# Optimization experiments

Hardware: AMD Instinct MI355X
Metric: run time of the kernel (lower is better)

## Reference

```python
import jax, jax.numpy as jnp
import numpy as np

EPS = 1e-8  # torch.nn.CosineSimilarity default eps


def _one_sided_chamfer(ex, ey):
    # ex: [N, D], ey: [M, D]
    # cosine(ex_i, ey_j) = <ex_i, ey_j> / (max(||ex_i||, eps) * max(||ey_j||, eps))
    nx = jnp.maximum(jnp.linalg.norm(ex, axis=-1, keepdims=True), EPS)  # [N,1]
    ny = jnp.maximum(jnp.linalg.norm(ey, axis=-1, keepdims=True), EPS)  # [M,1]
    exn = ex / nx
    eyn = ey / ny
    sims = jnp.einsum('nd,md->nm', exn, eyn)  # [N, M] cosine matrix
    return jnp.max(sims, axis=-1)  # row-wise max -> [N]


def setup_inputs() -> dict:
    key = jax.random.key(0)
    k1, k2 = jax.random.split(key)
    ex = jax.random.normal(k1, (8192, 768), dtype=jnp.float32)
    ey = jax.random.normal(k2, (8192, 768), dtype=jnp.float32)
    return {"ex": ex, "ey": ey}


def reference(ex, ey):
    return _one_sided_chamfer(ex, ey)
```

## Files before the change

### kernel.cpp

```cpp
#include <hip/hip_runtime.h>
#include <math.h>

#define NROWS 8192
#define KDIM  768
#define BM 128
#define BN 128
#define BKB 128
#define KTILES (KDIM / BKB)
#define NBC 4
#define NBCG (NROWS / BN / NBC)

typedef int i32x4 __attribute__((ext_vector_type(4)));

static __device__ __forceinline__ unsigned enc_f(float f) {
    unsigned x = __float_as_uint(f);
    return (x & 0x80000000u) ? ~x : (x | 0x80000000u);
}
static __device__ __forceinline__ float dec_f(unsigned u) {
    unsigned x = (u & 0x80000000u) ? (u ^ 0x80000000u) : ~u;
    return __uint_as_float(x);
}

__global__ __launch_bounds__(256) void normalize_quant_k(
        const float* __restrict__ ex, const float* __restrict__ ey,
        signed char* __restrict__ q, float* __restrict__ scales,
        unsigned* __restrict__ out) {
    if (blockIdx.x < NROWS / 256)
        out[blockIdx.x * 256 + threadIdx.x] = enc_f(-INFINITY);
    const int wave = threadIdx.x >> 6, lane = threadIdx.x & 63;
    const int grow = blockIdx.x * 4 + wave;
    const float* src = (grow < NROWS) ? ex : ey;
    const int row = grow & (NROWS - 1);
    const float4* xr = (const float4*)(src + (size_t)row * KDIM);
    float4 v[3];
    #pragma unroll
    for (int g = 0; g < 3; ++g) v[g] = xr[lane + g * 64];
    float ss = 0.f, am = 0.f;
    #pragma unroll
    for (int g = 0; g < 3; ++g) {
        ss += v[g].x * v[g].x + v[g].y * v[g].y + v[g].z * v[g].z + v[g].w * v[g].w;
        am = fmaxf(am, fmaxf(fmaxf(fabsf(v[g].x), fabsf(v[g].y)),
                             fmaxf(fabsf(v[g].z), fabsf(v[g].w))));
    }
    #pragma unroll
    for (int off = 32; off > 0; off >>= 1) {
        ss += __shfl_xor(ss, off);
        am = fmaxf(am, __shfl_xor(am, off));
    }
    const float scale = 1.0f / fmaxf(sqrtf(ss), 1e-8f);
    am = fmaxf(am * scale, 1e-12f);
    if (lane == 0) scales[grow] = am * (1.0f / 127.0f);
    const float si = scale * (127.0f / am);
    int* dr = (int*)(q + (size_t)grow * KDIM);
    #pragma unroll
    for (int g = 0; g < 3; ++g) {
        int qx = min(127, max(-127, __float2int_rn(v[g].x * si)));
        int qy = min(127, max(-127, __float2int_rn(v[g].y * si)));
        int qz = min(127, max(-127, __float2int_rn(v[g].z * si)));
        int qw = min(127, max(-127, __float2int_rn(v[g].w * si)));
        dr[lane + g * 64] = (qx & 0xff) | ((qy & 0xff) << 8) |
                            ((qz & 0xff) << 16) | ((qw & 0xff) << 24);
    }
}

__global__ __launch_bounds__(256, 4) void gemm_rowmax_i8_k(
        const signed char* __restrict__ A, const signed char* __restrict__ B,
        const float* __restrict__ sa, const float* __restrict__ sb,
        unsigned* __restrict__ out) {
    __shared__ signed char As[BM * BKB];
    __shared__ signed char Bs[BN * BKB];

    const int tid  = threadIdx.x;
    const int wave = tid >> 6, lane = tid & 63;
    const int br  = blockIdx.x >> 4;
    const int bcg = blockIdx.x & 15;

    const int srow   = lane >> 3;
    const int gchunk = (lane & 7) ^ srow;
    const int scol   = gchunk * 16;
    const signed char* aStage = A + (size_t)(br * BM + wave * 8 + srow) * KDIM + scol;
    signed char* lA = As + wave * 1024;
    signed char* lB = Bs + wave * 1024;

    const int wm = (wave >> 1) * 64, wn = (wave & 1) * 64;
    const int quad = lane >> 4, mrow = lane & 15;
    const int c0 = quad ^ (mrow & 7);
    const signed char* aBase = As + (wm + mrow) * BKB;
    const signed char* bBase = Bs + (wn + mrow) * BKB;
    const int row0 = br * BM + wm + quad * 4;

    #pragma unroll 1
    for (int bi = 0; bi < NBC; ++bi) {
        const int bc = bcg * NBC + bi;
        const signed char* bStage =
            B + (size_t)(bc * BN + wave * 8 + srow) * KDIM + scol;

        i32x4 acc[4][4] = {};

        #pragma unroll 1
        for (int kt = 0; kt < KTILES; ++kt) {
            __syncthreads();
            #pragma unroll
            for (int i = 0; i < 4; ++i) {
                __builtin_amdgcn_global_load_lds(
                    (const __attribute__((address_space(1))) void*)(aStage + kt * BKB + i * 24576),
                    (__attribute__((address_space(3))) void*)(lA + i * 4096), 16, 0, 0);
                __builtin_amdgcn_global_load_lds(
                    (const __attribute__((address_space(1))) void*)(bStage + kt * BKB + i * 24576),
                    (__attribute__((address_space(3))) void*)(lB + i * 4096), 16, 0, 0);
            }
            __syncthreads();

            #pragma unroll 1
            for (int ks = 0; ks < 2; ++ks) {
                const int ck = c0 ^ (ks << 2);
                i32x4 af[4], bfr[4];
                #pragma unroll
                for (int mi = 0; mi < 4; ++mi)
                    af[mi] = *(const i32x4*)(aBase + mi * 16 * BKB + ck * 16);
                #pragma unroll
                for (int ni = 0; ni < 4; ++ni)
                    bfr[ni] = *(const i32x4*)(bBase + ni * 16 * BKB + ck * 16);
                #pragma unroll
                for (int mi = 0; mi < 4; ++mi)
                    #pragma unroll
                    for (int ni = 0; ni < 4; ++ni)
                        acc[mi][ni] = __builtin_amdgcn_mfma_i32_16x16x64_i8(
                            af[mi], bfr[ni], acc[mi][ni], 0, 0, 0);
            }
        }

        float sbv[4];
        #pragma unroll
        for (int ni = 0; ni < 4; ++ni)
            sbv[ni] = sb[bc * BN + wn + ni * 16 + mrow];
        #pragma unroll
        for (int mi = 0; mi < 4; ++mi) {
            #pragma unroll
            for (int r = 0; r < 4; ++r) {
                float v = fmaxf(fmaxf((float)acc[mi][0][r] * sbv[0],
                                      (float)acc[mi][1][r] * sbv[1]),
                                fmaxf((float)acc[mi][2][r] * sbv[2],
                                      (float)acc[mi][3][r] * sbv[3]));
                v = fmaxf(v, __shfl_xor(v, 1));
                v = fmaxf(v, __shfl_xor(v, 2));
                v = fmaxf(v, __shfl_xor(v, 4));
                v = fmaxf(v, __shfl_xor(v, 8));
                if (mrow == 0) {
                    const int row = row0 + mi * 16 + r;
                    atomicMax(&out[row], enc_f(v * sa[row]));
                }
            }
        }
    }
}

__global__ void decode_out_k(unsigned* __restrict__ u) {
    int i = blockIdx.x * 256 + threadIdx.x;
    ((float*)u)[i] = dec_f(u[i]);
}

extern "C" void kernel_launch(void* const* d_in, const int* in_sizes, int n_in,
                              void* d_out, int out_size, void* d_ws, size_t ws_size,
                              hipStream_t stream) {
    (void)in_sizes; (void)n_in; (void)out_size; (void)ws_size;
    const float* ex = (const float*)d_in[0];
    const float* ey = (const float*)d_in[1];
    signed char* q = (signed char*)d_ws;
    float* scales  = (float*)(q + 2 * (size_t)NROWS * KDIM);
    unsigned* outu = (unsigned*)d_out;

    normalize_quant_k<<<(2 * NROWS) / 4, 256, 0, stream>>>(ex, ey, q, scales, outu);
    gemm_rowmax_i8_k<<<(NROWS / BM) * NBCG, 256, 0, stream>>>(
        q, q + (size_t)NROWS * KDIM, scales, scales + NROWS, outu);
    decode_out_k<<<NROWS / 256, 256, 0, stream>>>(outu);
}
```

Measured before the change: 158.0 us.

## Pre-swizzle int8 operands into MFMA fragment layout and load directly from global

The quantize kernel now writes int8 data in a tiled layout that matches the MFMA fragment order: 16-row groups, with each 64-byte k-chunk laid out lane-contiguous. The GEMM kernel drops LDS staging and both barriers per k-tile, and each wave reads its fragments straight from global memory with coalesced 16-byte loads. This removes the LDS round trip and the synchronisation cost. In exchange, operands shared across waves are loaded redundantly from global/L2 and there is no explicit prefetch, so load latency is exposed.

```diff
diff --git a/kernel.cpp b/kernel.cpp
--- a/kernel.cpp
+++ b/kernel.cpp
@@ -5,8 +5,8 @@
 #define KDIM  768
 #define BM 128
 #define BN 128
-#define BKB 128
-#define KTILES (KDIM / BKB)
+#define NCH 12
+#define GBYTES 12288
 #define NBC 4
 #define NBCG (NROWS / BN / NBC)
 
@@ -23,43 +23,51 @@
 
 __global__ __launch_bounds__(256) void normalize_quant_k(
         const float* __restrict__ ex, const float* __restrict__ ey,
-        signed char* __restrict__ q, float* __restrict__ scales,
+        signed char* __restrict__ qt, float* __restrict__ scales,
         unsigned* __restrict__ out) {
-    if (blockIdx.x < NROWS / 256)
-        out[blockIdx.x * 256 + threadIdx.x] = enc_f(-INFINITY);
+    const int b = blockIdx.x;
+    if (b < NROWS / 256)
+        out[b * 256 + threadIdx.x] = enc_f(-INFINITY);
     const int wave = threadIdx.x >> 6, lane = threadIdx.x & 63;
-    const int grow = blockIdx.x * 4 + wave;
-    const float* src = (grow < NROWS) ? ex : ey;
-    const int row = grow & (NROWS - 1);
-    const float4* xr = (const float4*)(src + (size_t)row * KDIM);
-    float4 v[3];
+    const int r_local = wave * 4 + (lane >> 4);
+    const int l16 = lane & 15;
+    const int grow = b * 16 + r_local;
+    const float* src = (b < 512) ? ex : ey;
+    const int Rl = ((b & 511) * 16 + r_local);
+    const float4* xr = (const float4*)(src + (size_t)Rl * KDIM);
+
+    float4 v[NCH];
     #pragma unroll
-    for (int g = 0; g < 3; ++g) v[g] = xr[lane + g * 64];
+    for (int rep = 0; rep < NCH; ++rep) v[rep] = xr[l16 + 16 * rep];
+
     float ss = 0.f, am = 0.f;
     #pragma unroll
-    for (int g = 0; g < 3; ++g) {
-        ss += v[g].x * v[g].x + v[g].y * v[g].y + v[g].z * v[g].z + v[g].w * v[g].w;
-        am = fmaxf(am, fmaxf(fmaxf(fabsf(v[g].x), fabsf(v[g].y)),
-                             fmaxf(fabsf(v[g].z), fabsf(v[g].w))));
+    for (int rep = 0; rep < NCH; ++rep) {
+        ss += v[rep].x * v[rep].x + v[rep].y * v[rep].y +
+              v[rep].z * v[rep].z + v[rep].w * v[rep].w;
+        am = fmaxf(am, fmaxf(fmaxf(fabsf(v[rep].x), fabsf(v[rep].y)),
+                             fmaxf(fabsf(v[rep].z), fabsf(v[rep].w))));
     }
     #pragma unroll
-    for (int off = 32; off > 0; off >>= 1) {
+    for (int off = 1; off < 16; off <<= 1) {
         ss += __shfl_xor(ss, off);
         am = fmaxf(am, __shfl_xor(am, off));
     }
     const float scale = 1.0f / fmaxf(sqrtf(ss), 1e-8f);
     am = fmaxf(am * scale, 1e-12f);
-    if (lane == 0) scales[grow] = am * (1.0f / 127.0f);
+    if (l16 == 0) scales[grow] = am * (1.0f / 127.0f);
     const float si = scale * (127.0f / am);
-    int* dr = (int*)(q + (size_t)grow * KDIM);
+
+    signed char* gbase = qt + (size_t)b * GBYTES
+                       + (l16 >> 2) * 256 + r_local * 16 + (l16 & 3) * 4;
     #pragma unroll
-    for (int g = 0; g < 3; ++g) {
-        int qx = min(127, max(-127, __float2int_rn(v[g].x * si)));
-        int qy = min(127, max(-127, __float2int_rn(v[g].y * si)));
-        int qz = min(127, max(-127, __float2int_rn(v[g].z * si)));
-        int qw = min(127, max(-127, __float2int_rn(v[g].w * si)));
-        dr[lane + g * 64] = (qx & 0xff) | ((qy & 0xff) << 8) |
-                            ((qz & 0xff) << 16) | ((qw & 0xff) << 24);
+    for (int rep = 0; rep < NCH; ++rep) {
+        int qx = min(127, max(-127, __float2int_rn(v[rep].x * si)));
+        int qy = min(127, max(-127, __float2int_rn(v[rep].y * si)));
+        int qz = min(127, max(-127, __float2int_rn(v[rep].z * si)));
+        int qw = min(127, max(-127, __float2int_rn(v[rep].w * si)));
+        *(int*)(gbase + rep * 1024) =
+            (qx & 0xff) | ((qy & 0xff) << 8) | ((qz & 0xff) << 16) | ((qw & 0xff) << 24);
     }
 }
 
@@ -67,73 +75,47 @@
         const signed char* __restrict__ A, const signed char* __restrict__ B,
         const float* __restrict__ sa, const float* __restrict__ sb,
         unsigned* __restrict__ out) {
-    __shared__ signed char As[BM * BKB];
-    __shared__ signed char Bs[BN * BKB];
-
     const int tid  = threadIdx.x;
     const int wave = tid >> 6, lane = tid & 63;
     const int br  = blockIdx.x >> 4;
     const int bcg = blockIdx.x & 15;
 
-    const int srow   = lane >> 3;
-    const int gchunk = (lane & 7) ^ srow;
-    const int scol   = gchunk * 16;
-    const signed char* aStage = A + (size_t)(br * BM + wave * 8 + srow) * KDIM + scol;
-    signed char* lA = As + wave * 1024;
-    signed char* lB = Bs + wave * 1024;
+    const int wgA = (wave >> 1) * 4;
+    const int wgB = (wave & 1) * 4;
+    const size_t laneoff = (size_t)lane * 16;
 
-    const int wm = (wave >> 1) * 64, wn = (wave & 1) * 64;
+    const signed char* aT = A + (size_t)(br * 8 + wgA) * GBYTES + laneoff;
     const int quad = lane >> 4, mrow = lane & 15;
-    const int c0 = quad ^ (mrow & 7);
-    const signed char* aBase = As + (wm + mrow) * BKB;
-    const signed char* bBase = Bs + (wn + mrow) * BKB;
-    const int row0 = br * BM + wm + quad * 4;
+    const int row0 = br * BM + wgA * 16 + quad * 4;
 
     #pragma unroll 1
     for (int bi = 0; bi < NBC; ++bi) {
         const int bc = bcg * NBC + bi;
-        const signed char* bStage =
-            B + (size_t)(bc * BN + wave * 8 + srow) * KDIM + scol;
+        const signed char* bT = B + (size_t)(bc * 8 + wgB) * GBYTES + laneoff;
 
         i32x4 acc[4][4] = {};
 
         #pragma unroll 1
-        for (int kt = 0; kt < KTILES; ++kt) {
-            __syncthreads();
+        for (int c = 0; c < NCH; ++c) {
+            i32x4 af[4], bfr[4];
             #pragma unroll
-            for (int i = 0; i < 4; ++i) {
-                __builtin_amdgcn_global_load_lds(
-                    (const __attribute__((address_space(1))) void*)(aStage + kt * BKB + i * 24576),
-                    (__attribute__((address_space(3))) void*)(lA + i * 4096), 16, 0, 0);
-                __builtin_amdgcn_global_load_lds(
-                    (const __attribute__((address_space(1))) void*)(bStage + kt * BKB + i * 24576),
-                    (__attribute__((address_space(3))) void*)(lB + i * 4096), 16, 0, 0);
-            }
-            __syncthreads();
-
-            #pragma unroll 1
-            for (int ks = 0; ks < 2; ++ks) {
-                const int ck = c0 ^ (ks << 2);
-                i32x4 af[4], bfr[4];
-                #pragma unroll
-                for (int mi = 0; mi < 4; ++mi)
-                    af[mi] = *(const i32x4*)(aBase + mi * 16 * BKB + ck * 16);
+            for (int mi = 0; mi < 4; ++mi)
+                af[mi] = *(const i32x4*)(aT + (size_t)mi * GBYTES + c * 1024);
+            #pragma unroll
+            for (int ni = 0; ni < 4; ++ni)
+                bfr[ni] = *(const i32x4*)(bT + (size_t)ni * GBYTES + c * 1024);
+            #pragma unroll
+            for (int mi = 0; mi < 4; ++mi)
                 #pragma unroll
                 for (int ni = 0; ni < 4; ++ni)
-                    bfr[ni] = *(const i32x4*)(bBase + ni * 16 * BKB + ck * 16);
-                #pragma unroll
-                for (int mi = 0; mi < 4; ++mi)
-                    #pragma unroll
-                    for (int ni = 0; ni < 4; ++ni)
-                        acc[mi][ni] = __builtin_amdgcn_mfma_i32_16x16x64_i8(
-                            af[mi], bfr[ni], acc[mi][ni], 0, 0, 0);
-            }
+                    acc[mi][ni] = __builtin_amdgcn_mfma_i32_16x16x64_i8(
+                        af[mi], bfr[ni], acc[mi][ni], 0, 0, 0);
         }
 
         float sbv[4];
         #pragma unroll
         for (int ni = 0; ni < 4; ++ni)
-            sbv[ni] = sb[bc * BN + wn + ni * 16 + mrow];
+            sbv[ni] = sb[bc * BN + wgB * 16 + ni * 16 + mrow];
         #pragma unroll
         for (int mi = 0; mi < 4; ++mi) {
             #pragma unroll
@@ -167,11 +149,11 @@
     const float* ex = (const float*)d_in[0];
     const float* ey = (const float*)d_in[1];
     signed char* q = (signed char*)d_ws;
-    float* scales  = (float*)(q + 2 * (size_t)NROWS * KDIM);
+    float* scales  = (float*)(q + 2 * (size_t)512 * GBYTES);
     unsigned* outu = (unsigned*)d_out;
 
-    normalize_quant_k<<<(2 * NROWS) / 4, 256, 0, stream>>>(ex, ey, q, scales, outu);
+    normalize_quant_k<<<1024, 256, 0, stream>>>(ex, ey, q, scales, outu);
     gemm_rowmax_i8_k<<<(NROWS / BM) * NBCG, 256, 0, stream>>>(
-        q, q + (size_t)NROWS * KDIM, scales, scales + NROWS, outu);
+        q, q + (size_t)512 * GBYTES, scales, scales + NROWS, outu);
     decode_out_k<<<NROWS / 256, 256, 0, stream>>>(outu);
 }
```

Measured after the change: 171.2 us. 1.08x slower.
